# Performance work log

Hardware: AMD Instinct MI355X
Metric: run time of the kernel (lower is better)

The kernel has to match this reference:

```python
import jax, jax.numpy as jnp
import numpy as np


def setup_inputs() -> dict:
    key = jax.random.key(0)
    k1, k2, k3 = jax.random.split(key, 3)
    B, T, D, H = 64, 512, 1024, 1024
    x = jax.random.normal(k1, (B, T, D), dtype=jnp.float32)
    state = jnp.zeros((B, H), dtype=jnp.float32)
    W = jax.random.normal(k2, (H, H), dtype=jnp.float32) / np.sqrt(H).astype(np.float32)
    U = jax.random.normal(k3, (D, H), dtype=jnp.float32) / np.sqrt(D).astype(np.float32)
    b = jnp.zeros((H,), dtype=jnp.float32)
    return {"x": x, "state": state, "W": W, "U": U, "b": b}


def reference(x, state, W, U, b):
    # x: (B, T, D) -> precompute input projection for all steps: (T, B, H)
    xU = jnp.einsum('btd,dh->tbh', x, U) + b

    def step(h, xu_t):
        h = jnp.tanh(xu_t + h @ W)
        return h, h

    final_state, outs = jax.lax.scan(step, state, xU)  # outs: (T, B, H)
    outs = jnp.transpose(outs, (1, 0, 2))  # (B, T, H)
    return outs, final_state
```

## Files before the change

kernel.cpp:

```cpp
#include <hip/hip_runtime.h>
#include <hip/hip_fp16.h>

typedef float  f4v __attribute__((ext_vector_type(4)));
typedef _Float16 h8v __attribute__((ext_vector_type(8)));
typedef _Float16 h4v __attribute__((ext_vector_type(4)));

#define B_ 64
#define T_ 512
#define H_ 1024

__global__ __launch_bounds__(256) void k_transpose_cvt(const float* __restrict__ src,
                                                       _Float16* __restrict__ dst) {
  __shared__ _Float16 tile[64][72];
  int r0 = blockIdx.y * 64, c0 = blockIdx.x * 64;
  int t = threadIdx.x;
  for (int i = 0; i < 4; ++i) {
    int r = i * 16 + (t >> 4);
    int c = (t & 15) * 4;
    f4v v = *reinterpret_cast<const f4v*>(src + (long)(r0 + r) * 1024 + c0 + c);
    tile[c + 0][r] = (_Float16)v.x;
    tile[c + 1][r] = (_Float16)v.y;
    tile[c + 2][r] = (_Float16)v.z;
    tile[c + 3][r] = (_Float16)v.w;
  }
  __syncthreads();
  for (int i = 0; i < 2; ++i) {
    int rr = i * 32 + (t >> 3);
    int cc = (t & 7) * 8;
    *reinterpret_cast<h8v*>(dst + (long)(c0 + rr) * 1024 + r0 + cc) =
        *reinterpret_cast<const h8v*>(&tile[rr][cc]);
  }
}

#define SWZG(r, kh) ((((r) * 64) + ((kh) * 2)) ^ (((r) & 3) << 4))

__global__ __launch_bounds__(256) void k_gemm_xu(const float* __restrict__ x,
                                                 const _Float16* __restrict__ Ut,
                                                 const float* __restrict__ bias,
                                                 float* __restrict__ out) {
  __shared__ __attribute__((aligned(16))) unsigned char Asm[128 * 32 * 2];
  __shared__ __attribute__((aligned(16))) unsigned char Bsm[128 * 32 * 2];
  int bid = blockIdx.x;
  int nt = bid & 7, mt = bid >> 3;
  int t = threadIdx.x;
  int row = t >> 1, kc = (t & 1) * 16;
  long gA = (long)(mt * 128 + row) * 1024 + kc;
  long gB = (long)(nt * 128 + row) * 1024 + kc;
  int wid = t >> 6, lane = t & 63;
  int wr = (wid >> 1) * 64, wc = (wid & 1) * 64;
  int l15 = lane & 15, khi = (lane >> 4) * 8;

  f4v acc[4][4];
  for (int i = 0; i < 4; ++i)
    for (int j = 0; j < 4; ++j) acc[i][j] = (f4v){0.f, 0.f, 0.f, 0.f};

  f4v ra[4];
  h8v rb[2];
  {
    const float* ap = x + gA;
    ra[0] = *(const f4v*)(ap);     ra[1] = *(const f4v*)(ap + 4);
    ra[2] = *(const f4v*)(ap + 8); ra[3] = *(const f4v*)(ap + 12);
    const _Float16* bp = Ut + gB;
    rb[0] = *(const h8v*)(bp);     rb[1] = *(const h8v*)(bp + 8);
  }
  for (int kt = 0; kt < 32; ++kt) {
    h8v ah0, ah1;
    for (int j = 0; j < 4; ++j) {
      ah0[j]     = (_Float16)ra[0][j];
      ah0[j + 4] = (_Float16)ra[1][j];
      ah1[j]     = (_Float16)ra[2][j];
      ah1[j + 4] = (_Float16)ra[3][j];
    }
    *(h8v*)(Asm + SWZG(row, kc))     = ah0;
    *(h8v*)(Asm + SWZG(row, kc + 8)) = ah1;
    *(h8v*)(Bsm + SWZG(row, kc))     = rb[0];
    *(h8v*)(Bsm + SWZG(row, kc + 8)) = rb[1];
    __syncthreads();
    if (kt < 31) {
      const float* ap = x + gA + (kt + 1) * 32;
      ra[0] = *(const f4v*)(ap);     ra[1] = *(const f4v*)(ap + 4);
      ra[2] = *(const f4v*)(ap + 8); ra[3] = *(const f4v*)(ap + 12);
      const _Float16* bp = Ut + gB + (kt + 1) * 32;
      rb[0] = *(const h8v*)(bp);     rb[1] = *(const h8v*)(bp + 8);
    }
    h8v af[4], bf[4];
    for (int mi = 0; mi < 4; ++mi)
      af[mi] = *(const h8v*)(Asm + SWZG(wr + mi * 16 + l15, khi));
    for (int ni = 0; ni < 4; ++ni)
      bf[ni] = *(const h8v*)(Bsm + SWZG(wc + ni * 16 + l15, khi));
    for (int mi = 0; mi < 4; ++mi)
      for (int ni = 0; ni < 4; ++ni)
        acc[mi][ni] = __builtin_amdgcn_mfma_f32_16x16x32_f16(af[mi], bf[ni], acc[mi][ni], 0, 0, 0);
    __syncthreads();
  }
  int coff = nt * 128 + wc, roff = mt * 128 + wr;
  for (int ni = 0; ni < 4; ++ni) {
    int col = coff + ni * 16 + l15;
    float bb = bias[col];
    for (int mi = 0; mi < 4; ++mi) {
      int rbase = roff + mi * 16 + (lane >> 4) * 4;
      for (int j = 0; j < 4; ++j)
        out[(long)(rbase + j) * 1024 + col] = acc[mi][ni][j] + bb;
    }
  }
}

#define SWZS(r, kh) ((((r) * 2048) + ((kh) * 2)) ^ (((r) & 7) << 4))

__global__ __launch_bounds__(256) void k_scan(const float* __restrict__ state,
                                              float* __restrict__ out,
                                              const _Float16* __restrict__ Wt,
                                              unsigned* __restrict__ ctr) {
  extern __shared__ __attribute__((aligned(16))) unsigned char smem[];
  unsigned char* Wl = smem;
  unsigned char* Hl0 = smem + 65536;
  __shared__ int fastflag;
  int t = threadIdx.x;
  int bid = blockIdx.x;
  int cl = bid & 7;
  int mm = bid >> 3;
  int lane = t & 63;

  unsigned* stepc = ctr + cl * 32;
  unsigned* gbar  = ctr + 512;

  {
    int r = t >> 3, c8 = t & 7;
    const _Float16* wsrc = Wt + (long)(mm * 32 + r) * 1024;
    for (int j = 0; j < 16; ++j) {
      int kh = (c8 + 8 * j) * 8;
      *(h8v*)(Wl + SWZS(r, kh)) = *(const h8v*)(wsrc + kh);
    }
  }

  if (t == 0) {
    unsigned* tst = ctr + 1024 + bid * 32;
    unsigned val = 0xC0FFEE00u + (unsigned)bid;
    asm volatile("global_store_dword %0, %1, off\n\ts_waitcnt vmcnt(0)"
                 :: "v"(tst), "v"(val) : "memory");
    __hip_atomic_fetch_add(gbar, 1u, __ATOMIC_RELAXED, __HIP_MEMORY_SCOPE_AGENT);
    while (__hip_atomic_load(gbar, __ATOMIC_RELAXED, __HIP_MEMORY_SCOPE_AGENT) < 256u)
      __builtin_amdgcn_s_sleep(2);
  }
  __syncthreads();
  if (t < 64) {
    bool ok = true;
    if (lane < 32) {
      int peer = lane * 8 + cl;
      unsigned* ps = ctr + 1024 + peer * 32;
      unsigned v;
      asm volatile("global_load_dword %0, %1, off\n\ts_waitcnt vmcnt(0)"
                   : "=v"(v) : "v"(ps) : "memory");
      ok = (v == 0xC0FFEE00u + (unsigned)peer);
    }
    unsigned long long m = __ballot(ok);
    if (t == 0) fastflag = (m == ~0ULL);
  }
  __syncthreads();
  const bool fastm = (fastflag != 0);

  int wid = t >> 6;
  int srow = t >> 5, slane = t & 31;
  long b = cl * 8 + srow;
  int l15 = lane & 15, khi8 = (lane >> 4) * 8;
  int arow = lane & 7;
  int bro = wid * 16 + l15;
  int hi = lane >> 4;
  int gcol = mm * 32 + wid * 16 + l15;
  bool prod = (wid < 2) && (hi < 2);

  for (int step = 0; step < T_; ++step) {
    unsigned char* Hb = Hl0 + (step & 1) * 16384;

    float xuv[4];
    long addr0 = 0;
    if (prod) {
      addr0 = ((long)(cl * 8 + hi * 4) * T_ + step) * 1024 + gcol;
#pragma unroll
      for (int j = 0; j < 4; ++j) xuv[j] = out[addr0 + (long)j * T_ * 1024];
    }

    if (step == 0) {
      const float* hp0 = state + b * 1024 + slane * 4;
#pragma unroll
      for (int j = 0; j < 8; ++j) {
        f4v v = *(const f4v*)(hp0 + 128 * j);
        h4v hv = {(_Float16)v.x, (_Float16)v.y, (_Float16)v.z, (_Float16)v.w};
        *(h4v*)(Hb + SWZS(srow, (slane + 32 * j) * 4)) = hv;
      }
    } else {
      if (t == 0) {
        unsigned tgt = 32u * (unsigned)step;
        while (__hip_atomic_load(stepc, __ATOMIC_RELAXED, __HIP_MEMORY_SCOPE_AGENT) < tgt)
          __builtin_amdgcn_s_sleep(1);
      }
      __syncthreads();

      const float* hrow = out + (b * T_ + (step - 1)) * 1024;
      if (fastm) {
#pragma unroll
        for (int j = 0; j < 8; ++j) {
          int c0 = (slane + 32 * j) * 4;
          if ((c0 >> 5) == mm) continue;
          f4v v = *(const f4v*)(hrow + c0);
          h4v hv = {(_Float16)v.x, (_Float16)v.y, (_Float16)v.z, (_Float16)v.w};
          *(h4v*)(Hb + SWZS(srow, c0)) = hv;
        }
      } else {
        const float* hp = hrow + slane * 4;
        f4v w0, w1, w2, w3, w4, w5, w6, w7;
        asm volatile(
            "global_load_dwordx4 %0, %8, off sc0 sc1\n\t"
            "global_load_dwordx4 %1, %8, off offset:512 sc0 sc1\n\t"
            "global_load_dwordx4 %2, %8, off offset:1024 sc0 sc1\n\t"
            "global_load_dwordx4 %3, %8, off offset:1536 sc0 sc1\n\t"
            "global_load_dwordx4 %4, %8, off offset:2048 sc0 sc1\n\t"
            "global_load_dwordx4 %5, %8, off offset:2560 sc0 sc1\n\t"
            "global_load_dwordx4 %6, %8, off offset:3072 sc0 sc1\n\t"
            "global_load_dwordx4 %7, %8, off offset:3584 sc0 sc1\n\t"
            "s_waitcnt vmcnt(0)"
            : "=&v"(w0), "=&v"(w1), "=&v"(w2), "=&v"(w3),
              "=&v"(w4), "=&v"(w5), "=&v"(w6), "=&v"(w7)
            : "v"(hp)
            : "memory");
        f4v wv[8] = {w0, w1, w2, w3, w4, w5, w6, w7};
#pragma unroll
        for (int j = 0; j < 8; ++j) {
          int c0 = (slane + 32 * j) * 4;
          h4v hv = {(_Float16)wv[j][0], (_Float16)wv[j][1],
                    (_Float16)wv[j][2], (_Float16)wv[j][3]};
          *(h4v*)(Hb + SWZS(srow, c0)) = hv;
        }
      }
    }
    __syncthreads();

    if (wid < 2) {
      f4v ac0 = (f4v){0.f, 0.f, 0.f, 0.f}, ac1 = ac0, ac2 = ac0, ac3 = ac0;
#pragma unroll
      for (int s = 0; s < 32; s += 4) {
        int k0 = s * 32 + khi8, k1 = k0 + 32, k2 = k0 + 64, k3 = k0 + 96;
        h8v af0 = *(const h8v*)(Hb + SWZS(arow, k0));
        h8v bf0 = *(const h8v*)(Wl + SWZS(bro, k0));
        h8v af1 = *(const h8v*)(Hb + SWZS(arow, k1));
        h8v bf1 = *(const h8v*)(Wl + SWZS(bro, k1));
        h8v af2 = *(const h8v*)(Hb + SWZS(arow, k2));
        h8v bf2 = *(const h8v*)(Wl + SWZS(bro, k2));
        h8v af3 = *(const h8v*)(Hb + SWZS(arow, k3));
        h8v bf3 = *(const h8v*)(Wl + SWZS(bro, k3));
        ac0 = __builtin_amdgcn_mfma_f32_16x16x32_f16(af0, bf0, ac0, 0, 0, 0);
        ac1 = __builtin_amdgcn_mfma_f32_16x16x32_f16(af1, bf1, ac1, 0, 0, 0);
        ac2 = __builtin_amdgcn_mfma_f32_16x16x32_f16(af2, bf2, ac2, 0, 0, 0);
        ac3 = __builtin_amdgcn_mfma_f32_16x16x32_f16(af3, bf3, ac3, 0, 0, 0);
      }
      f4v acc = (ac0 + ac1) + (ac2 + ac3);
      if (hi < 2) {
        float v0 = tanhf(acc[0] + xuv[0]);
        float v1 = tanhf(acc[1] + xuv[1]);
        float v2 = tanhf(acc[2] + xuv[2]);
        float v3 = tanhf(acc[3] + xuv[3]);
        float* p0 = out + addr0;
        float* p1 = p0 + (long)T_ * 1024;
        float* p2 = p1 + (long)T_ * 1024;
        float* p3 = p2 + (long)T_ * 1024;
        if (fastm) {
          p0[0] = v0; p1[0] = v1; p2[0] = v2; p3[0] = v3;
        } else {
          asm volatile(
              "global_store_dword %0, %4, off sc0 sc1\n\t"
              "global_store_dword %1, %5, off sc0 sc1\n\t"
              "global_store_dword %2, %6, off sc0 sc1\n\t"
              "global_store_dword %3, %7, off sc0 sc1\n\t"
              "s_waitcnt vmcnt(0)"
              :: "v"(p0), "v"(p1), "v"(p2), "v"(p3),
                 "v"(v0), "v"(v1), "v"(v2), "v"(v3)
              : "memory");
        }
        if (step < T_ - 1) {
          unsigned char* Hn = Hl0 + ((step + 1) & 1) * 16384;
          int cb = gcol & ~3, co = (gcol & 3) * 2;
          int r0r = hi * 4;
          *(_Float16*)(Hn + SWZS(r0r + 0, cb) + co) = (_Float16)v0;
          *(_Float16*)(Hn + SWZS(r0r + 1, cb) + co) = (_Float16)v1;
          *(_Float16*)(Hn + SWZS(r0r + 2, cb) + co) = (_Float16)v2;
          *(_Float16*)(Hn + SWZS(r0r + 3, cb) + co) = (_Float16)v3;
        }
        if (step == T_ - 1) {
          long r = (long)cl * 8 + hi * 4;
          float* q = out + (long)B_ * T_ * 1024 + r * 1024 + gcol;
          q[0] = v0; q[1024] = v1; q[2048] = v2; q[3072] = v3;
        }
      }
    }

    if (prod) {
      asm volatile("s_waitcnt vmcnt(0)" ::: "memory");
    }
    __syncthreads();
    if (t == 0) {
      __hip_atomic_fetch_add(stepc, 1u, __ATOMIC_RELAXED, __HIP_MEMORY_SCOPE_AGENT);
    }
  }
}

extern "C" void kernel_launch(void* const* d_in, const int* in_sizes, int n_in,
                              void* d_out, int out_size, void* d_ws, size_t ws_size,
                              hipStream_t stream) {
  const float* x     = (const float*)d_in[0];
  const float* state = (const float*)d_in[1];
  const float* W     = (const float*)d_in[2];
  const float* U     = (const float*)d_in[3];
  const float* bias  = (const float*)d_in[4];
  float* out = (float*)d_out;
  unsigned char* ws = (unsigned char*)d_ws;

  _Float16* Ut = (_Float16*)ws;
  _Float16* Wt = (_Float16*)(ws + (1u << 21));
  unsigned* ctr = (unsigned*)(ws + (1u << 22));

  hipMemsetAsync(ctr, 0, 40960, stream);

  k_transpose_cvt<<<dim3(16, 16), 256, 0, stream>>>(U, Ut);
  k_transpose_cvt<<<dim3(16, 16), 256, 0, stream>>>(W, Wt);
  k_gemm_xu<<<2048, 256, 0, stream>>>(x, Ut, bias, out);

  hipFuncSetAttribute((const void*)k_scan, hipFuncAttributeMaxDynamicSharedMemorySize, 98304);
  void* args[] = {(void*)&state, (void*)&out, (void*)&Wt, (void*)&ctr};
  hipLaunchCooperativeKernel((void*)k_scan, dim3(256), dim3(256), args, 98304, stream);
}
```

Before: 1.762 ms.

## Replace per-step atomic counter with per-block flag array polled by vector loads

On the fast path, each block now signals step completion by storing its step index into its own slot of a per-cluster flag array, instead of doing an atomic add on a shared counter. Waiters poll all 32 flags with eight dwordx4 loads and a min-reduction. The startup probe is extended to a two-phase visibility test with a bad-count reduction to decide whether the fast path is safe. The aim is to remove atomic contention and serialization in the per-step inter-block barrier, at the cost of more polling traffic and a longer startup check.

```diff
diff --git a/kernel.cpp b/kernel.cpp
--- a/kernel.cpp
+++ b/kernel.cpp
@@ -4,6 +4,7 @@
 typedef float  f4v __attribute__((ext_vector_type(4)));
 typedef _Float16 h8v __attribute__((ext_vector_type(8)));
 typedef _Float16 h4v __attribute__((ext_vector_type(4)));
+typedef unsigned uv4 __attribute__((ext_vector_type(4)));
 
 #define B_ 64
 #define T_ 512
@@ -121,8 +122,13 @@
   int mm = bid >> 3;
   int lane = t & 63;
 
-  unsigned* stepc = ctr + cl * 32;
-  unsigned* gbar  = ctr + 512;
+  unsigned* stepc  = ctr + cl * 32;
+  unsigned* gbar0  = ctr + 512;
+  unsigned* gbar1  = ctr + 544;
+  unsigned* gbar2  = ctr + 576;
+  unsigned* badc   = ctr + 640 + cl * 32;
+  unsigned* flagsF = ctr + 1024 + cl * 32;
+  unsigned* tst    = ctr + 2048 + bid * 32;
 
   {
     int r = t >> 3, c8 = t & 7;
@@ -134,27 +140,51 @@
   }
 
   if (t == 0) {
-    unsigned* tst = ctr + 1024 + bid * 32;
-    unsigned val = 0xC0FFEE00u + (unsigned)bid;
+    unsigned vA = 0xA0000000u + (unsigned)bid;
     asm volatile("global_store_dword %0, %1, off\n\ts_waitcnt vmcnt(0)"
-                 :: "v"(tst), "v"(val) : "memory");
-    __hip_atomic_fetch_add(gbar, 1u, __ATOMIC_RELAXED, __HIP_MEMORY_SCOPE_AGENT);
-    while (__hip_atomic_load(gbar, __ATOMIC_RELAXED, __HIP_MEMORY_SCOPE_AGENT) < 256u)
+                 :: "v"(tst), "v"(vA) : "memory");
+    __hip_atomic_fetch_add(gbar0, 1u, __ATOMIC_RELAXED, __HIP_MEMORY_SCOPE_AGENT);
+    while (__hip_atomic_load(gbar0, __ATOMIC_RELAXED, __HIP_MEMORY_SCOPE_AGENT) < 256u)
       __builtin_amdgcn_s_sleep(2);
   }
   __syncthreads();
-  if (t < 64) {
-    bool ok = true;
-    if (lane < 32) {
-      int peer = lane * 8 + cl;
-      unsigned* ps = ctr + 1024 + peer * 32;
-      unsigned v;
-      asm volatile("global_load_dword %0, %1, off\n\ts_waitcnt vmcnt(0)"
-                   : "=v"(v) : "v"(ps) : "memory");
-      ok = (v == 0xC0FFEE00u + (unsigned)peer);
-    }
-    unsigned long long m = __ballot(ok);
-    if (t == 0) fastflag = (m == ~0ULL);
+  bool okA = true;
+  unsigned* ps = nullptr;
+  if (t < 32) {
+    int peer = t * 8 + cl;
+    ps = ctr + 2048 + peer * 32;
+    unsigned v;
+    asm volatile("global_load_dword %0, %1, off sc0\n\ts_waitcnt vmcnt(0)"
+                 : "=v"(v) : "v"(ps) : "memory");
+    okA = (v == 0xA0000000u + (unsigned)(t * 8 + cl));
+  }
+  __syncthreads();
+  if (t == 0) {
+    unsigned vB = 0xB0000000u + (unsigned)bid;
+    asm volatile("global_store_dword %0, %1, off\n\ts_waitcnt vmcnt(0)"
+                 :: "v"(tst), "v"(vB) : "memory");
+    __hip_atomic_fetch_add(gbar1, 1u, __ATOMIC_RELAXED, __HIP_MEMORY_SCOPE_AGENT);
+    while (__hip_atomic_load(gbar1, __ATOMIC_RELAXED, __HIP_MEMORY_SCOPE_AGENT) < 256u)
+      __builtin_amdgcn_s_sleep(2);
+  }
+  __syncthreads();
+  bool okB = true;
+  if (t < 32) {
+    unsigned v;
+    asm volatile("global_load_dword %0, %1, off sc0\n\ts_waitcnt vmcnt(0)"
+                 : "=v"(v) : "v"(ps) : "memory");
+    okB = (v == 0xB0000000u + (unsigned)(t * 8 + cl));
+  }
+  if (t < 32 && !(okA && okB)) {
+    __hip_atomic_fetch_add(badc, 1u, __ATOMIC_RELAXED, __HIP_MEMORY_SCOPE_AGENT);
+  }
+  asm volatile("s_waitcnt vmcnt(0)" ::: "memory");
+  __syncthreads();
+  if (t == 0) {
+    __hip_atomic_fetch_add(gbar2, 1u, __ATOMIC_RELAXED, __HIP_MEMORY_SCOPE_AGENT);
+    while (__hip_atomic_load(gbar2, __ATOMIC_RELAXED, __HIP_MEMORY_SCOPE_AGENT) < 256u)
+      __builtin_amdgcn_s_sleep(2);
+    fastflag = (__hip_atomic_load(badc, __ATOMIC_RELAXED, __HIP_MEMORY_SCOPE_AGENT) == 0u);
   }
   __syncthreads();
   const bool fastm = (fastflag != 0);
@@ -190,9 +220,38 @@
       }
     } else {
       if (t == 0) {
-        unsigned tgt = 32u * (unsigned)step;
-        while (__hip_atomic_load(stepc, __ATOMIC_RELAXED, __HIP_MEMORY_SCOPE_AGENT) < tgt)
-          __builtin_amdgcn_s_sleep(1);
+        unsigned tgt = (unsigned)step;
+        if (fastm) {
+          for (;;) {
+            uv4 f0, f1, f2, f3, f4, f5, f6, f7;
+            asm volatile(
+                "global_load_dwordx4 %0, %8, off sc0\n\t"
+                "global_load_dwordx4 %1, %8, off offset:16 sc0\n\t"
+                "global_load_dwordx4 %2, %8, off offset:32 sc0\n\t"
+                "global_load_dwordx4 %3, %8, off offset:48 sc0\n\t"
+                "global_load_dwordx4 %4, %8, off offset:64 sc0\n\t"
+                "global_load_dwordx4 %5, %8, off offset:80 sc0\n\t"
+                "global_load_dwordx4 %6, %8, off offset:96 sc0\n\t"
+                "global_load_dwordx4 %7, %8, off offset:112 sc0\n\t"
+                "s_waitcnt vmcnt(0)"
+                : "=&v"(f0), "=&v"(f1), "=&v"(f2), "=&v"(f3),
+                  "=&v"(f4), "=&v"(f5), "=&v"(f6), "=&v"(f7)
+                : "v"(flagsF)
+                : "memory");
+            uv4 m0 = __builtin_elementwise_min(__builtin_elementwise_min(f0, f1),
+                                               __builtin_elementwise_min(f2, f3));
+            uv4 m1 = __builtin_elementwise_min(__builtin_elementwise_min(f4, f5),
+                                               __builtin_elementwise_min(f6, f7));
+            uv4 m = __builtin_elementwise_min(m0, m1);
+            unsigned mn = m.x < m.y ? m.x : m.y;
+            unsigned mn2 = m.z < m.w ? m.z : m.w;
+            if ((mn < mn2 ? mn : mn2) >= tgt) break;
+          }
+        } else {
+          unsigned tgt32 = 32u * (unsigned)step;
+          while (__hip_atomic_load(stepc, __ATOMIC_RELAXED, __HIP_MEMORY_SCOPE_AGENT) < tgt32)
+            __builtin_amdgcn_s_sleep(1);
+        }
       }
       __syncthreads();
 
@@ -298,7 +357,13 @@
     }
     __syncthreads();
     if (t == 0) {
-      __hip_atomic_fetch_add(stepc, 1u, __ATOMIC_RELAXED, __HIP_MEMORY_SCOPE_AGENT);
+      if (fastm) {
+        unsigned e = (unsigned)(step + 1);
+        asm volatile("global_store_dword %0, %1, off"
+                     :: "v"(flagsF + mm), "v"(e) : "memory");
+      } else {
+        __hip_atomic_fetch_add(stepc, 1u, __ATOMIC_RELAXED, __HIP_MEMORY_SCOPE_AGENT);
+      }
     }
   }
 }
```

Result: no change. 1.783 ms (+1.2%).
